# Performance work log

Measured on AMD Instinct MI355X. Metric: run time of the kernel, lower is better.

## Reference

```python
import jax, jax.numpy as jnp
import numpy as np
from jax import lax

KS = 3       # kernel_size
PAD = 1      # padding
STRIDE = 1
DIL = 2      # dilation (scales adaptive offsets)
N = KS * KS
DN = ('NCHW', 'OIHW', 'NCHW')


def _conv(x, w, stride, padding):
    return lax.conv_general_dilated(x, w, (stride, stride),
                                    [(padding, padding), (padding, padding)],
                                    dimension_numbers=DN)


def _deform_forward(x, w_p, b_p, w_m, w_ad, w_conv):
    B, C, H, W = x.shape
    offset = _conv(x, w_p, STRIDE, 1) + b_p[None, :, None, None]      # (B,2N,H,W)
    ad_base = 1.0 - jax.nn.sigmoid(_conv(x, w_ad, STRIDE, 1))         # (B,KS,H,W)
    ad = jnp.tile(ad_base, (1, 2 * KS, 1, 1)) * DIL                   # (B,2N,H,W)
    ad_m = jnp.tile((ad_base - 0.5) * 2.0, (1, KS, 1, 1)) * DIL       # (B,N,H,W)
    m = jax.nn.sigmoid(_conv(x, w_m, STRIDE, 1))                      # (B,N,H,W)

    # kernel relative offsets p_n: (1,2N,1,1)
    r = jnp.arange(-(KS - 1) // 2, (KS - 1) // 2 + 1, dtype=x.dtype)
    pnx, pny = jnp.meshgrid(r, r, indexing='ij')
    p_n = jnp.concatenate([pnx.ravel(), pny.ravel()])[None, :, None, None]
    # base sampling coords p_0: (1,2N,H,W), offset by 1 to match zero padding
    ix = jnp.arange(1, H * STRIDE + 1, STRIDE, dtype=x.dtype)
    iy = jnp.arange(1, W * STRIDE + 1, STRIDE, dtype=x.dtype)
    p0x, p0y = jnp.meshgrid(ix, iy, indexing='ij')
    p_0 = jnp.concatenate([jnp.broadcast_to(p0x, (1, N, H, W)),
                           jnp.broadcast_to(p0y, (1, N, H, W))], axis=1)

    p = p_0 + p_n + offset + ad * p_n                                  # (B,2N,H,W)
    p = p.transpose(0, 2, 3, 1)                                        # (B,H,W,2N)

    xp = jnp.pad(x, ((0, 0), (0, 0), (PAD, PAD), (PAD, PAD)))         # (B,C,Hp,Wp)
    Hp, Wp = H + 2 * PAD, W + 2 * PAD

    q_lt = jnp.floor(p)
    q_rb = q_lt + 1.0

    def clampxy(q):
        return jnp.concatenate([jnp.clip(q[..., :N], 0, Hp - 1),
                                jnp.clip(q[..., N:], 0, Wp - 1)], -1).astype(jnp.int32)

    q_lt = clampxy(q_lt)
    q_rb = clampxy(q_rb)
    q_lb = jnp.concatenate([q_lt[..., :N], q_rb[..., N:]], -1)
    q_rt = jnp.concatenate([q_rb[..., :N], q_lt[..., N:]], -1)

    # out-of-range mask (detached); snap those points to floor, then clamp
    mask = jnp.concatenate([
        (p[..., :N] < PAD) | (p[..., :N] > Hp - 1 - PAD),
        (p[..., N:] < PAD) | (p[..., N:] > Wp - 1 - PAD)], -1).astype(p.dtype)
    mask = lax.stop_gradient(mask)
    p = p * (1 - mask) + jnp.floor(p) * mask
    p = jnp.concatenate([jnp.clip(p[..., :N], 0, Hp - 1),
                         jnp.clip(p[..., N:], 0, Wp - 1)], -1)

    def g(q, sx, sy):  # bilinear weights
        qx = q[..., :N].astype(p.dtype)
        qy = q[..., N:].astype(p.dtype)
        return (1 + sx * (qx - p[..., :N])) * (1 + sy * (qy - p[..., N:]))

    g_lt = g(q_lt, 1, 1)
    g_rb = g(q_rb, -1, -1)
    g_lb = g(q_lb, 1, -1)
    g_rt = g(q_rt, -1, 1)

    x_flat = xp.reshape(B, C, Hp * Wp)
    L = H * W * N

    def gather(q):
        idx = (q[..., :N] * Wp + q[..., N:]).reshape(B, 1, L)
        idx = jnp.broadcast_to(idx, (B, C, L))
        return jnp.take_along_axis(x_flat, idx, axis=2).reshape(B, C, H, W, N)

    x_off = (g_lt[:, None] * gather(q_lt) + g_rb[:, None] * gather(q_rb)
             + g_lb[:, None] * gather(q_lb) + g_rt[:, None] * gather(q_rt))

    # modulation scaled by adaptive term
    mm = (m * ad_m).transpose(0, 2, 3, 1)[:, None]                     # (B,1,H,W,N)
    x_off = x_off * mm

    # (B,C,H,W,ks*ks) -> (B,C,H*ks,W*ks)
    x_off = x_off.reshape(B, C, H, W, KS, KS).transpose(0, 1, 2, 4, 3, 5)
    x_off = x_off.reshape(B, C, H * KS, W * KS)
    return _conv(x_off, w_conv, KS, 0)                                 # (B,Cout,H,W)


def setup_inputs() -> dict:
    key = jax.random.key(0)
    ks = jax.random.split(key, 6)
    C_in, C_out = 64, 64
    x = jax.random.normal(ks[0], (2, C_in, 128, 128), jnp.float32)
    w_p = jax.random.normal(ks[1], (2 * N, C_in, 3, 3), jnp.float32) * 0.01
    b_p = jax.random.normal(ks[2], (2 * N,), jnp.float32) * 0.01
    w_m = jax.random.normal(ks[3], (N, C_in, 3, 3), jnp.float32) * 0.05
    w_ad = jax.random.normal(ks[4], (KS, C_in, 3, 3), jnp.float32) * 0.05
    w_conv = jax.random.normal(ks[5], (C_out, C_in, KS, KS), jnp.float32) / np.sqrt(C_in * N).astype(np.float32)
    return {"x": x, "w_p": w_p, "b_p": b_p, "w_m": w_m, "w_ad": w_ad, "w_conv": w_conv}


def reference(x, w_p, b_p, w_m, w_ad, w_conv):
    return _deform_forward(x, w_p, b_p, w_m, w_ad, w_conv)
```

## Files before the change

kernel.cpp:

```cpp
#include <hip/hip_runtime.h>
#include <hip/hip_fp16.h>
#include <math.h>

#define H 128
#define W 128
#define BATCH 2

typedef short short8 __attribute__((ext_vector_type(8)));
typedef float f32x4 __attribute__((ext_vector_type(4)));
typedef float f32x16 __attribute__((ext_vector_type(16)));

#define BPLANE 1081600
#define PLANE  2163200
#define XS_M   PLANE
#define WC_OFF (2 * PLANE)
#define WM_OFF (WC_OFF + 36864)
#define WM_PLANE 18432
#define META_OFF (WM_OFF + 2 * WM_PLANE)

__device__ __forceinline__ unsigned f2bf_u(float f) {
    union { float f; unsigned u; } v; v.f = f;
    return (v.u + 0x7FFFu + ((v.u >> 16) & 1u)) >> 16;
}
__device__ __forceinline__ float bfbits2f(unsigned lo16) {
    union { unsigned u; float f; } v; v.u = lo16 << 16;
    return v.f;
}
__device__ __forceinline__ float bfs2f(short s) {
    union { unsigned u; float f; } v; v.u = ((unsigned)(unsigned short)s) << 16;
    return v.f;
}
__device__ __forceinline__ void split2(float v, unsigned& h, unsigned& m) {
    h = f2bf_u(v);
    float r1 = v - bfbits2f(h);
    m = f2bf_u(r1);
}

__global__ __launch_bounds__(512) void prep_kernel(
    const float* __restrict__ x, const float* __restrict__ w_p,
    const float* __restrict__ w_m, const float* __restrict__ w_ad,
    const float* __restrict__ w_conv, unsigned short* __restrict__ ws)
{
    const int blk = blockIdx.x, t = threadIdx.x;
    if (blk < 264) {
        int xcd = blk & 7, q = blk >> 3;
        int sub = xcd & 3, b = xcd >> 2;
        int hrow;
        if (sub == 0)      { if (q > 32) return; hrow = q; }
        else if (sub == 3) { if (q > 32) return; hrow = 97 + q; }
        else               { if (q > 31) return; hrow = sub * 32 + 1 + q; }
        size_t rb = ((size_t)b * 16900 + hrow * 130) * 32;
        unsigned* uh = (unsigned*)ws + rb;
        unsigned* um = (unsigned*)(ws + XS_M) + rb;
        if (hrow == 0 || hrow == 129) {
            for (int f = t; f < 4160; f += 512) { uh[f] = 0; um[f] = 0; }
            return;
        }
        __shared__ float s[64 * 129];
        int h = hrow - 1;
        for (int f = t; f < 64 * 32; f += 512) {
            int ci = f >> 5, w4 = f & 31;
            *(float4*)&s[ci * 129 + w4 * 4] =
                *(const float4*)&x[((size_t)(b * 64 + ci) * 128 + h) * 128 + w4 * 4];
        }
        __syncthreads();
        for (int f = t; f < 128 * 8; f += 512) {
            int w = f >> 3, g = f & 7;
            unsigned hv[4], mv[4];
            #pragma unroll
            for (int p = 0; p < 4; ++p) {
                int cip = g * 4 + p;
                unsigned h0, m0, h1, m1;
                split2(s[(2 * cip) * 129 + w], h0, m0);
                split2(s[(2 * cip + 1) * 129 + w], h1, m1);
                hv[p] = h0 | (h1 << 16);
                mv[p] = m0 | (m1 << 16);
            }
            int o = (w + 1) * 32 + g * 4;
            *(uint4*)&uh[o] = make_uint4(hv[0], hv[1], hv[2], hv[3]);
            *(uint4*)&um[o] = make_uint4(mv[0], mv[1], mv[2], mv[3]);
        }
        if (t < 32)      { uh[t] = 0; um[t] = 0; }
        else if (t < 64) { int o = 129 * 32 + (t - 32); uh[o] = 0; um[o] = 0; }
    } else if (blk < 282) {
        int q = (blk - 264) * 512 + t;
        int e = q * 4;
        int j = e & 15, co = (e >> 4) & 63, kk = e >> 10;
        int klin = kk * 16 + j;
        int n = klin >> 6, ci = klin & 63;
        const float* src = w_conv + co * 576 + n;
        ushort4 r;
        r.x = (unsigned short)f2bf_u(src[(ci + 0) * 9]);
        r.y = (unsigned short)f2bf_u(src[(ci + 1) * 9]);
        r.z = (unsigned short)f2bf_u(src[(ci + 2) * 9]);
        r.w = (unsigned short)f2bf_u(src[(ci + 3) * 9]);
        *(ushort4*)(ws + WC_OFF + e) = r;
    } else {
        int q = (blk - 282) * 512 + t;
        int oc = q / 576, k = q % 576;
        int s = k >> 6, ci = k & 63;
        float v = 0.f;
        if (oc < 18)      v = w_p[oc * 576 + ci * 9 + s];
        else if (oc < 21) v = w_ad[(oc - 18) * 576 + ci * 9 + s];
        else if (oc < 30) v = w_m[(oc - 21) * 576 + ci * 9 + s];
        unsigned hh, mm; split2(v, hh, mm);
        ws[WM_OFF + q] = (unsigned short)hh;
        ws[WM_OFF + WM_PLANE + q] = (unsigned short)mm;
    }
}

__global__ __launch_bounds__(512, 2) void meta_kernel(
    const float* __restrict__ b_p, const unsigned short* __restrict__ wsu,
    float* __restrict__ meta)
{
    __shared__ __align__(16) unsigned short s_w[64 * 584];
    const int t = threadIdx.x;
    const int d = blockIdx.x;
    const int l = (d & 7) * 32 + (d >> 3);
    const int b = l >> 7, i = l & 127;

    #pragma unroll
    for (int it = 0; it < 9; ++it) {
        int chunk = it * 512 + t;
        int r = chunk / 72, c8 = chunk % 72;
        *(short8*)(s_w + r * 584 + c8 * 8) =
            *(const short8*)(wsu + WM_OFF + chunk * 8);
    }
    __syncthreads();

    const int wv = t >> 6, lane = t & 63, lr = lane & 15, lg = lane >> 4;
    const int px = wv * 16 + lr;
    const unsigned short* xsb = wsu + (size_t)b * BPLANE;

    f32x4 aA0 = {0,0,0,0}, aB0 = {0,0,0,0}, aA1 = {0,0,0,0}, aB1 = {0,0,0,0};
    #pragma unroll
    for (int kk = 0; kk < 18; ++kk) {
        const int s = kk >> 1;
        const unsigned short* bp = xsb + ((i + s / 3) * 130 + (px + s % 3)) * 64
                                   + ((kk & 1) << 5) + lg * 8;
        short8 bh = *(const short8*)(bp);
        short8 bm = *(const short8*)(bp + XS_M);
        const unsigned short* w0 = s_w + lr * 584 + kk * 32 + lg * 8;
        short8 ah0 = *(const short8*)(w0);
        short8 am0 = *(const short8*)(w0 + 32 * 584);
        const unsigned short* w1 = w0 + 16 * 584;
        short8 ah1 = *(const short8*)(w1);
        short8 am1 = *(const short8*)(w1 + 32 * 584);
        aA0 = __builtin_amdgcn_mfma_f32_16x16x32_bf16(ah0, bh, aA0, 0, 0, 0);
        aB0 = __builtin_amdgcn_mfma_f32_16x16x32_bf16(ah0, bm, aB0, 0, 0, 0);
        aA0 = __builtin_amdgcn_mfma_f32_16x16x32_bf16(am0, bh, aA0, 0, 0, 0);
        aA1 = __builtin_amdgcn_mfma_f32_16x16x32_bf16(ah1, bh, aA1, 0, 0, 0);
        aB1 = __builtin_amdgcn_mfma_f32_16x16x32_bf16(ah1, bm, aB1, 0, 0, 0);
        aA1 = __builtin_amdgcn_mfma_f32_16x16x32_bf16(am1, bh, aA1, 0, 0, 0);
    }

    float* mb = meta + (((size_t)b * 128 + i) * 128 + px) * 32;
    {
        const float4 bq = *(const float4*)(b_p + lg * 4);
        f32x4 o0;
        o0[0] = aA0[0] + aB0[0] + bq.x;
        o0[1] = aA0[1] + aB0[1] + bq.y;
        o0[2] = aA0[2] + aB0[2] + bq.z;
        o0[3] = aA0[3] + aB0[3] + bq.w;
        *(f32x4*)(mb + lg * 4) = o0;
    }
    {
        f32x4 o1;
        #pragma unroll
        for (int r = 0; r < 4; ++r) {
            int oc = 16 + lg * 4 + r;
            float v = aA1[r] + aB1[r];
            if (oc < 18)      v += b_p[oc];
            else if (oc < 21) v = 1.f - 1.f / (1.f + expf(-v));
            else              v = 1.f / (1.f + expf(-v));
            o1[r] = v;
        }
        *(f32x4*)(mb + 16 + lg * 4) = o1;
    }
}

__global__ __launch_bounds__(512, 8) void deform_kernel(
    const unsigned short* __restrict__ wsu, const float* __restrict__ meta,
    float* __restrict__ out)
{
    __shared__ __align__(16) char smem[40832];
    unsigned short* s_valb = (unsigned short*)smem;
    __half2* s_gh = (__half2*)(smem + 37376);
    int* s_idxp = (int*)(smem + 39680);

    const int t = threadIdx.x;
    const int d = blockIdx.x;
    const int l = (d & 7) * 128 + (d >> 3);
    const int jb = l & 3, i = (l >> 2) & 127, b = l >> 9;
    const int j0 = jb * 32;

    if (t < 288) {
        int pix = t / 9, n = t % 9;
        int ki = n / 3, kj = n % 3;
        const float* mrow = meta + (((size_t)b * 128 + i) * 128 + j0 + pix) * 32;
        float adb  = mrow[18 + kj];
        float offx = mrow[n];
        float offy = mrow[9 + n];
        float msig = mrow[21 + n];
        float pnx = (float)(ki - 1), pny = (float)(kj - 1);
        float pxc = (float)(i + 1)        + pnx + offx + 2.f * adb * pnx;
        float pyc = (float)(j0 + pix + 1) + pny + offy + 2.f * adb * pny;

        float flx = floorf(pxc), fly = floorf(pyc);
        int ix0 = (int)fminf(fmaxf(flx,       0.f), 129.f);
        int ix1 = (int)fminf(fmaxf(flx + 1.f, 0.f), 129.f);
        int iy0 = (int)fminf(fmaxf(fly,       0.f), 129.f);
        int iy1 = (int)fminf(fmaxf(fly + 1.f, 0.f), 129.f);

        float ptx = (pxc < 1.f || pxc > 128.f) ? flx : pxc;
        float pty = (pyc < 1.f || pyc > 128.f) ? fly : pyc;
        ptx = fminf(fmaxf(ptx, 0.f), 129.f);
        pty = fminf(fmaxf(pty, 0.f), 129.f);

        float wxl = 1.f + (float)ix0 - ptx;
        float wxr = 1.f - ((float)ix1 - ptx);
        float wyl = 1.f + (float)iy0 - pty;
        float wyr = 1.f - ((float)iy1 - pty);

        float mm = msig * (adb - 0.5f) * 4.f;

        s_gh[t * 2 + 0] = __floats2half2_rn(wxl * wyl * mm, wxr * wyr * mm);
        s_gh[t * 2 + 1] = __floats2half2_rn(wxl * wyr * mm, wxr * wyl * mm);
        s_idxp[t] = ix0 | (ix1 << 8) | (iy0 << 16) | (iy1 << 24);
    }
    __syncthreads();

    const unsigned short* xsb = wsu + (size_t)b * BPLANE;
    #define GATHER(TASK) do {                                                     \
        int task = (TASK);                                                        \
        int n = task >> 8, pix = (task >> 3) & 31, cig = task & 7;                \
        int pk = s_idxp[pix * 9 + n];                                             \
        int ix0 = pk & 255, ix1 = (pk >> 8) & 255;                                \
        int iy0 = (pk >> 16) & 255, iy1 = (pk >> 24) & 255;                       \
        const unsigned short* base = xsb + cig * 8;                               \
        short8 v00 = *(const short8*)(base + (ix0 * 130 + iy0) * 64);             \
        short8 v11 = *(const short8*)(base + (ix1 * 130 + iy1) * 64);             \
        short8 v01 = *(const short8*)(base + (ix0 * 130 + iy1) * 64);             \
        short8 v10 = *(const short8*)(base + (ix1 * 130 + iy0) * 64);             \
        float2 g01 = __half22float2(s_gh[(pix * 9 + n) * 2 + 0]);                 \
        float2 g23 = __half22float2(s_gh[(pix * 9 + n) * 2 + 1]);                 \
        unsigned po[4];                                                           \
        _Pragma("unroll")                                                         \
        for (int jp = 0; jp < 4; ++jp) {                                          \
            float e0 = g01.x * bfs2f(v00[2 * jp])     + g01.y * bfs2f(v11[2 * jp])\
                     + g23.x * bfs2f(v01[2 * jp])     + g23.y * bfs2f(v10[2 * jp]);\
            float e1 = g01.x * bfs2f(v00[2 * jp + 1]) + g01.y * bfs2f(v11[2 * jp + 1])\
                     + g23.x * bfs2f(v01[2 * jp + 1]) + g23.y * bfs2f(v10[2 * jp + 1]);\
            po[jp] = f2bf_u(e0) | (f2bf_u(e1) << 16);                             \
        }                                                                         \
        *(uint4*)(s_valb + pix * 584 + n * 64 + cig * 8)                          \
            = make_uint4(po[0], po[1], po[2], po[3]);                             \
    } while (0)

    #pragma unroll
    for (int it = 0; it < 4; ++it) GATHER(t + it * 512);
    if (t < 256) GATHER(t + 2048);
    #undef GATHER
    __syncthreads();

    {
        const int w = t >> 6, lane = t & 63;
        const int ch = w & 1, kq = w >> 1;
        const int colA = lane & 31, hi = lane >> 5;
        const unsigned short* wa = wsu + WC_OFF + ((kq * 9) * 64 + ch * 32 + colA) * 16 + hi * 8;
        const unsigned short* vb = s_valb + colA * 584 + (kq * 9) * 16 + hi * 8;
        f32x16 acc = {0,0,0,0,0,0,0,0,0,0,0,0,0,0,0,0};
        #pragma unroll
        for (int s = 0; s < 9; ++s) {
            short8 a   = *(const short8*)(wa + s * 1024);
            short8 bfr = *(const short8*)(vb + s * 16);
            acc = __builtin_amdgcn_mfma_f32_32x32x16_bf16(a, bfr, acc, 0, 0, 0);
        }
        __syncthreads();
        float* sp = (float*)smem;
        #pragma unroll
        for (int r = 0; r < 16; ++r)
            sp[(w * 16 + r) * 65 + lane] = acc[r];
        __syncthreads();
        int ch2 = t >> 8, e = t & 255;
        int lane2 = e & 63, rq = e >> 6;
        #pragma unroll
        for (int q = 0; q < 4; ++q) {
            int reg = rq * 4 + q;
            float v = sp[((0 + ch2) * 16 + reg) * 65 + lane2]
                    + sp[((2 + ch2) * 16 + reg) * 65 + lane2]
                    + sp[((4 + ch2) * 16 + reg) * 65 + lane2]
                    + sp[((6 + ch2) * 16 + reg) * 65 + lane2];
            int col = lane2 & 31;
            int row = (reg & 3) + 8 * (reg >> 2) + 4 * (lane2 >> 5);
            int co = ch2 * 32 + row;
            out[(((size_t)b * 64 + co) * 128 + i) * 128 + j0 + col] = v;
        }
    }
}

extern "C" void kernel_launch(void* const* d_in, const int* in_sizes, int n_in,
                              void* d_out, int out_size, void* d_ws, size_t ws_size,
                              hipStream_t stream) {
    const float* x      = (const float*)d_in[0];
    const float* w_p    = (const float*)d_in[1];
    const float* b_p    = (const float*)d_in[2];
    const float* w_m    = (const float*)d_in[3];
    const float* w_ad   = (const float*)d_in[4];
    const float* w_conv = (const float*)d_in[5];
    float* outp = (float*)d_out;
    unsigned short* ws = (unsigned short*)d_ws;
    float* meta_f = (float*)(ws + META_OFF);

    prep_kernel<<<318, 512, 0, stream>>>(x, w_p, w_m, w_ad, w_conv, ws);
    meta_kernel<<<256, 512, 0, stream>>>(b_p, ws, meta_f);
    deform_kernel<<<1024, 512, 0, stream>>>(ws, meta_f, outp);
}
```

Baseline: 34.29 us.

## Use 32x32x16 MFMA with split-K across waves in meta conv kernel

Rewrites the offset/mask/adaptive conv kernel to use 32x32x16 bf16 MFMA tiles, reads pre-swizzled weights straight from global memory instead of staging them in LDS, and splits the K dimension across wave pairs. The partial sums are reduced through shared memory before the sigmoid and bias epilogue. The weight prep layout is changed to match the new A-operand fragment order. This cuts MFMA instruction count and LDS weight staging, at the cost of an LDS reduction pass and scalar (non-vector) meta stores.

```diff
diff --git a/kernel.cpp b/kernel.cpp
--- a/kernel.cpp
+++ b/kernel.cpp
@@ -97,8 +97,9 @@
         *(ushort4*)(ws + WC_OFF + e) = r;
     } else {
         int q = (blk - 282) * 512 + t;
-        int oc = q / 576, k = q % 576;
-        int s = k >> 6, ci = k & 63;
+        int oc = (q >> 4) & 31, j = q & 15, kk = q >> 9;
+        int klin = kk * 16 + j;
+        int s = klin >> 6, ci = klin & 63;
         float v = 0.f;
         if (oc < 18)      v = w_p[oc * 576 + ci * 9 + s];
         else if (oc < 21) v = w_ad[(oc - 18) * 576 + ci * 9 + s];
@@ -113,69 +114,54 @@
     const float* __restrict__ b_p, const unsigned short* __restrict__ wsu,
     float* __restrict__ meta)
 {
-    __shared__ __align__(16) unsigned short s_w[64 * 584];
+    __shared__ __align__(16) float s_part[8 * 16 * 65];
     const int t = threadIdx.x;
     const int d = blockIdx.x;
     const int l = (d & 7) * 32 + (d >> 3);
     const int b = l >> 7, i = l & 127;
-
+    const unsigned short* xsb = wsu + (size_t)b * BPLANE;
+
+    const int w = t >> 6, lane = t & 63;
+    const int colA = lane & 31, hi = lane >> 5;
+    const int pt = w >> 1, kh = w & 1;
+    const int px = pt * 32 + colA;
+
+    f32x16 accA = {0,0,0,0,0,0,0,0,0,0,0,0,0,0,0,0};
+    f32x16 accB = {0,0,0,0,0,0,0,0,0,0,0,0,0,0,0,0};
     #pragma unroll
-    for (int it = 0; it < 9; ++it) {
-        int chunk = it * 512 + t;
-        int r = chunk / 72, c8 = chunk % 72;
-        *(short8*)(s_w + r * 584 + c8 * 8) =
-            *(const short8*)(wsu + WM_OFF + chunk * 8);
-    }
+    for (int it = 0; it < 18; ++it) {
+        int kk = kh * 18 + it;
+        int s = kk >> 2;
+        int sr = s / 3, sc = s - sr * 3;
+        const unsigned short* bp = xsb + ((i + sr) * 130 + (px + sc)) * 64
+                                   + (kk & 3) * 16 + hi * 8;
+        const unsigned short* ap = wsu + WM_OFF + (kk * 32 + colA) * 16 + hi * 8;
+        short8 ah = *(const short8*)ap;
+        short8 am = *(const short8*)(ap + WM_PLANE);
+        short8 bh = *(const short8*)bp;
+        short8 bm = *(const short8*)(bp + XS_M);
+        accA = __builtin_amdgcn_mfma_f32_32x32x16_bf16(ah, bh, accA, 0, 0, 0);
+        accB = __builtin_amdgcn_mfma_f32_32x32x16_bf16(am, bh, accB, 0, 0, 0);
+        accB = __builtin_amdgcn_mfma_f32_32x32x16_bf16(ah, bm, accB, 0, 0, 0);
+    }
+    #pragma unroll
+    for (int r = 0; r < 16; ++r)
+        s_part[(w * 16 + r) * 65 + lane] = accA[r] + accB[r];
     __syncthreads();
 
-    const int wv = t >> 6, lane = t & 63, lr = lane & 15, lg = lane >> 4;
-    const int px = wv * 16 + lr;
-    const unsigned short* xsb = wsu + (size_t)b * BPLANE;
-
-    f32x4 aA0 = {0,0,0,0}, aB0 = {0,0,0,0}, aA1 = {0,0,0,0}, aB1 = {0,0,0,0};
-    #pragma unroll
-    for (int kk = 0; kk < 18; ++kk) {
-        const int s = kk >> 1;
-        const unsigned short* bp = xsb + ((i + s / 3) * 130 + (px + s % 3)) * 64
-                                   + ((kk & 1) << 5) + lg * 8;
-        short8 bh = *(const short8*)(bp);
-        short8 bm = *(const short8*)(bp + XS_M);
-        const unsigned short* w0 = s_w + lr * 584 + kk * 32 + lg * 8;
-        short8 ah0 = *(const short8*)(w0);
-        short8 am0 = *(const short8*)(w0 + 32 * 584);
-        const unsigned short* w1 = w0 + 16 * 584;
-        short8 ah1 = *(const short8*)(w1);
-        short8 am1 = *(const short8*)(w1 + 32 * 584);
-        aA0 = __builtin_amdgcn_mfma_f32_16x16x32_bf16(ah0, bh, aA0, 0, 0, 0);
-        aB0 = __builtin_amdgcn_mfma_f32_16x16x32_bf16(ah0, bm, aB0, 0, 0, 0);
-        aA0 = __builtin_amdgcn_mfma_f32_16x16x32_bf16(am0, bh, aA0, 0, 0, 0);
-        aA1 = __builtin_amdgcn_mfma_f32_16x16x32_bf16(ah1, bh, aA1, 0, 0, 0);
-        aB1 = __builtin_amdgcn_mfma_f32_16x16x32_bf16(ah1, bm, aB1, 0, 0, 0);
-        aA1 = __builtin_amdgcn_mfma_f32_16x16x32_bf16(am1, bh, aA1, 0, 0, 0);
-    }
-
-    float* mb = meta + (((size_t)b * 128 + i) * 128 + px) * 32;
-    {
-        const float4 bq = *(const float4*)(b_p + lg * 4);
-        f32x4 o0;
-        o0[0] = aA0[0] + aB0[0] + bq.x;
-        o0[1] = aA0[1] + aB0[1] + bq.y;
-        o0[2] = aA0[2] + aB0[2] + bq.z;
-        o0[3] = aA0[3] + aB0[3] + bq.w;
-        *(f32x4*)(mb + lg * 4) = o0;
-    }
-    {
-        f32x4 o1;
-        #pragma unroll
-        for (int r = 0; r < 4; ++r) {
-            int oc = 16 + lg * 4 + r;
-            float v = aA1[r] + aB1[r];
+    for (int o = t; o < 4096; o += 512) {
+        int oc = o & 31, px2 = o >> 5;
+        if (oc < 30) {
+            int pt2 = px2 >> 5, col = px2 & 31;
+            int lane2 = col + ((oc >> 2) & 1) * 32;
+            int reg = (oc & 3) + 4 * (oc >> 3);
+            float v = s_part[((pt2 * 2 + 0) * 16 + reg) * 65 + lane2]
+                    + s_part[((pt2 * 2 + 1) * 16 + reg) * 65 + lane2];
             if (oc < 18)      v += b_p[oc];
             else if (oc < 21) v = 1.f - 1.f / (1.f + expf(-v));
             else              v = 1.f / (1.f + expf(-v));
-            o1[r] = v;
-        }
-        *(f32x4*)(mb + 16 + lg * 4) = o1;
+            meta[(((size_t)b * 128 + i) * 128 + px2) * 32 + oc] = v;
+        }
     }
 }
 
```

After: 38.67 us. 12.8% more time.
